# Performance work log

Hardware: AMD Instinct MI355X
Metric: run time of the kernel (lower is better)

The kernel has to match this reference:

```python
import jax, jax.numpy as jnp
import numpy as np

B, T, D, H, OUT = 4096, 48, 59, 256, 1


def _uni(k, shape, fan_in):
    s = 1.0 / np.sqrt(fan_in)
    return jax.random.uniform(k, shape, jnp.float32, -s, s)


def setup_inputs() -> dict:
    key = jax.random.key(0)
    ks = jax.random.split(key, 16)
    return {
        "x": jax.random.normal(ks[0], (B, T, D), jnp.float32),
        "mask": (jax.random.uniform(ks[1], (B, T, D)) < 0.7).astype(jnp.float32),
        "deltas": jax.random.uniform(ks[2], (B, T, D), jnp.float32) * 5.0,
        "last_obs": jax.random.normal(ks[3], (B, D), jnp.float32),
        "h": jax.random.normal(ks[4], (B, H), jnp.float32) * 0.1,
        "medians": jnp.zeros((D,), jnp.float32),  # medians_df=None -> zeros
        # Decay temp_decay_h (non-diag)
        "W_dh": _uni(ks[5], (H, D), D), "b_dh": jnp.zeros((H,), jnp.float32),
        # Decay temp_decay_x (diag, input==output)
        "W_dx": _uni(ks[6], (D, D), D), "b_dx": jnp.zeros((D,), jnp.float32),
        # hist: Linear(H, D)
        "hist_W": _uni(ks[7], (D, H), H), "hist_b": jnp.zeros((D,), jnp.float32),
        "feat_W": _uni(ks[8], (D, D), D), "feat_b": jnp.zeros((D,), jnp.float32),
        # weight_combine: Linear(2D, D)
        "wcomb_W": _uni(ks[9], (D, 2 * D), 2 * D), "wcomb_b": jnp.zeros((D,), jnp.float32),
        # Decay_obs linear (D, D)
        "wobs_W": _uni(ks[10], (D, D), D), "wobs_b": jnp.zeros((D,), jnp.float32),
        # GRUCell(2D, H)
        "W_ih": _uni(ks[11], (3 * H, 2 * D), 2 * D),
        "W_hh": _uni(ks[12], (3 * H, H), H),
        "b_ih": jnp.zeros((3 * H,), jnp.float32),
        "b_hh": jnp.zeros((3 * H,), jnp.float32),
        # classification: Linear(H, OUT)
        "cls_W": _uni(ks[13], (OUT, H), H), "cls_b": jnp.zeros((OUT,), jnp.float32),
    }


def reference(x, mask, deltas, last_obs, h, medians,
              W_dh, b_dh, W_dx, b_dx, hist_W, hist_b, feat_W, feat_b,
              wcomb_W, wcomb_b, wobs_W, wobs_b,
              W_ih, W_hh, b_ih, b_hh, cls_W, cls_b):
    Dn = x.shape[-1]
    Hn = h.shape[-1]
    eye = jnp.eye(Dn, dtype=x.dtype)

    # Decay_obs: sign-gated tanh weighting of (deltas - medians)
    dd = deltas - medians[None, None, :]
    wd = jnp.einsum('btd,ed->bte', dd, wobs_W) + wobs_b
    # relu(wd) + relu(-wd) == |wd|
    decay_factor = 0.5 * (1.0 - jnp.tanh(jnp.sign(dd) * jnp.abs(wd)))  # [B,T,D]

    dx_diag = jnp.diagonal(W_dx)          # diag decay: W * eye
    feat_Wm = feat_W * (1.0 - eye)

    def step(h, ins):
        x_t, m_t, d_t = ins               # each [B,D]
        gamma_h = jnp.exp(-jax.nn.relu(d_t @ W_dh.T + b_dh))   # [B,H]
        h = h * gamma_h
        x_h = h @ hist_W.T + hist_b                              # history estimate [B,D]
        x_r = m_t * x_t + (1.0 - m_t) * x_h                      # complemented input
        xu = x_r @ feat_Wm.T + feat_b
        gamma_x = jnp.exp(-jax.nn.relu(d_t * dx_diag + b_dx))    # diag decay [B,D]
        beta = jax.nn.sigmoid(
            jnp.concatenate([gamma_x, m_t], axis=-1) @ wcomb_W.T + wcomb_b)
        x_comb = beta * xu + (1.0 - beta) * x_h
        loss_t = jnp.sum(jnp.abs(x_t - x_comb) * m_t) / (jnp.sum(m_t) + 1e-5)
        x_imp_t = m_t * x_t + (1.0 - m_t) * x_comb
        # GRUCell with input concat([x_imp_t, m_t])
        gi = jnp.concatenate([x_imp_t, m_t], axis=-1) @ W_ih.T + b_ih
        gh = h @ W_hh.T + b_hh
        r = jax.nn.sigmoid(gi[:, :Hn] + gh[:, :Hn])
        z = jax.nn.sigmoid(gi[:, Hn:2 * Hn] + gh[:, Hn:2 * Hn])
        n = jnp.tanh(gi[:, 2 * Hn:] + r * gh[:, 2 * Hn:])
        h_new = (1.0 - z) * n + z * h
        return h_new, (x_imp_t, h_new, loss_t)

    xs = (x.transpose(1, 0, 2), mask.transpose(1, 0, 2), deltas.transpose(1, 0, 2))
    h_last, (x_imp, hs, losses) = jax.lax.scan(step, h, xs)
    x_imp = x_imp.transpose(1, 0, 2)          # [B,T,D]
    hidden_states = hs.transpose(1, 0, 2)     # [B,T,H]
    x_loss = jnp.sum(losses)
    y_out = h_last @ cls_W.T + cls_b          # dropout = identity at eval
    y_score = jax.nn.sigmoid(y_out)
    return x_imp, x_loss, hidden_states, y_out, y_score, decay_factor
```

## Files before the change

kernel.cpp:

```cpp
#include <hip/hip_runtime.h>
#include <math.h>

#define BATCH 4096
#define TT 48
#define DDIM 59
#define HHID 256
#define RR 16
#define NWG (BATCH/RR)
#define NTHR 512

typedef _Float16 f16;
typedef _Float16 f16x8 __attribute__((ext_vector_type(8)));
typedef float    f32x4 __attribute__((ext_vector_type(4)));

static constexpr size_t N_XIMP   = (size_t)BATCH*TT*DDIM;
static constexpr size_t OFF_LOSS = N_XIMP;
static constexpr size_t OFF_HS   = OFF_LOSS + 1;
static constexpr size_t N_HS     = (size_t)BATCH*TT*HHID;
static constexpr size_t OFF_YOUT = OFF_HS + N_HS;
static constexpr size_t OFF_YSC  = OFF_YOUT + BATCH;
static constexpr size_t OFF_DEC  = OFF_YSC + BATCH;

static constexpr size_t WOFF_GRU  = 0;
static constexpr size_t WOFF_DH   = 294912;
static constexpr size_t WOFF_HIST = 311296;
static constexpr size_t WOFF_FEAT = 327680;
static constexpr size_t WOFF_WC   = 331776;

__device__ __forceinline__ float sigm(float v){ return 1.f/(1.f+expf(-v)); }

__global__ __launch_bounds__(256) void decay_kernel(
    const float* __restrict__ deltas, const float* __restrict__ medians,
    const float* __restrict__ wobs_W, const float* __restrict__ wobs_b,
    float* __restrict__ out_decay)
{
  __shared__ float sW[DDIM][60];
  __shared__ float sb[64], smed[64];
  __shared__ float sdd[16][60];
  const int tid = threadIdx.x;
  for (int idx = tid; idx < DDIM*DDIM; idx += 256){
    int e = idx/DDIM, d = idx - e*DDIM;
    sW[e][d] = wobs_W[idx];
  }
  if (tid < DDIM){ sb[tid] = wobs_b[tid]; smed[tid] = medians[tid]; }
  __syncthreads();
  const size_t row0 = (size_t)blockIdx.x * 16;
  for (int idx = tid; idx < 16*DDIM; idx += 256){
    int r = idx/DDIM, d = idx - r*DDIM;
    sdd[r][d] = deltas[(row0+r)*DDIM + d] - smed[d];
  }
  __syncthreads();
  for (int idx = tid; idx < 16*DDIM; idx += 256){
    int r = idx/DDIM, e = idx - r*DDIM;
    float acc = sb[e];
    for (int d = 0; d < DDIM; d++) acc += sdd[r][d]*sW[e][d];
    float dd = sdd[r][e];
    float sg = (dd > 0.f) ? 1.f : ((dd < 0.f) ? -1.f : 0.f);
    out_decay[(row0+r)*DDIM + e] = 0.5f*(1.f - tanhf(sg*fabsf(acc)));
  }
}

__global__ __launch_bounds__(256) void conv_kernel(
    const float* __restrict__ W_dh, const float* __restrict__ hist_W,
    const float* __restrict__ feat_W, const float* __restrict__ wcomb_W,
    const float* __restrict__ W_ih, const float* __restrict__ W_hh,
    f16* __restrict__ ws)
{
  const int g  = blockIdx.x*4 + (threadIdx.x >> 6);
  const int l  = threadIdx.x & 63;
  const int nl = l & 15;
  const int kh = (l >> 4) * 8;
  f16x8 out;
  if (g < 576){
    int jb = g/36, s = g - jb*36;
    if (s < 24){
      int gate = s/12, kt = s - gate*12;
      int row  = gate*256 + jb*16 + nl;
      #pragma unroll
      for (int e = 0; e < 8; e++){
        int k = kt*32 + kh + e;
        float v = (k < 256) ? W_hh[(size_t)row*256 + k]
                : (k < 374) ? W_ih[(size_t)row*118 + (k-256)] : 0.f;
        out[e] = (f16)v;
      }
    } else if (s < 32){
      int kt = s - 24, row = 512 + jb*16 + nl;
      #pragma unroll
      for (int e = 0; e < 8; e++){
        int k = kt*32 + kh + e;
        out[e] = (f16)W_hh[(size_t)row*256 + k];
      }
    } else {
      int kt = s - 32, row = 512 + jb*16 + nl;
      #pragma unroll
      for (int e = 0; e < 8; e++){
        int k = kt*32 + kh + e;
        out[e] = (f16)((k < 118) ? W_ih[(size_t)row*118 + k] : 0.f);
      }
    }
    *(f16x8*)&ws[WOFF_GRU + (size_t)g*512 + l*8] = out;
  } else if (g < 608){
    int i = g - 576, nt = i >> 1, kt = i & 1;
    int row = nt*16 + nl;
    #pragma unroll
    for (int e = 0; e < 8; e++){
      int k = kt*32 + kh + e;
      out[e] = (f16)((k < 59) ? W_dh[(size_t)row*59 + k] : 0.f);
    }
    *(f16x8*)&ws[WOFF_DH + (size_t)i*512 + l*8] = out;
  } else if (g < 640){
    int i = g - 608, nt = i >> 3, kt = i & 7;
    int n = nt*16 + nl;
    #pragma unroll
    for (int e = 0; e < 8; e++){
      int k = kt*32 + kh + e;
      out[e] = (f16)((n < 59) ? hist_W[(size_t)n*256 + k] : 0.f);
    }
    *(f16x8*)&ws[WOFF_HIST + (size_t)i*512 + l*8] = out;
  } else if (g < 648){
    int i = g - 640, nt = i >> 1, kt = i & 1;
    int n = nt*16 + nl;
    #pragma unroll
    for (int e = 0; e < 8; e++){
      int k = kt*32 + kh + e;
      out[e] = (f16)((n < 59 && k < 59 && k != n) ? feat_W[(size_t)n*59 + k] : 0.f);
    }
    *(f16x8*)&ws[WOFF_FEAT + (size_t)i*512 + l*8] = out;
  } else {
    int i = g - 648, nt = i >> 2, kt = i & 3;
    int n = nt*16 + nl;
    #pragma unroll
    for (int e = 0; e < 8; e++){
      int k = kt*32 + kh + e;
      out[e] = (f16)((n < 59 && k < 118) ? wcomb_W[(size_t)n*118 + k] : 0.f);
    }
    *(f16x8*)&ws[WOFF_WC + (size_t)i*512 + l*8] = out;
  }
}

__global__ __launch_bounds__(NTHR, 1) void seq_kernel(
    const float* __restrict__ x, const float* __restrict__ mask,
    const float* __restrict__ deltas, const float* __restrict__ h0,
    const float* __restrict__ b_dh, const float* __restrict__ W_dx,
    const float* __restrict__ b_dx, const float* __restrict__ hist_b,
    const float* __restrict__ feat_b, const float* __restrict__ wcomb_b,
    const float* __restrict__ b_ih, const float* __restrict__ b_hh,
    const f16* __restrict__ wb,
    float* __restrict__ out_ximp, float* __restrict__ out_hs,
    float* __restrict__ ws_num, float* __restrict__ ws_den)
{
  __shared__ f16 Acat[16*392];
  __shared__ f16 Ad  [16*72];
  __shared__ f16 Axr [16*72];
  __shared__ f16 Agm [16*136];
  __shared__ float ssx[16*60], ssm[16*60], ssd[16*60];
  __shared__ float sxh[16*60], sxu[16*60], sbt[16*60];
  __shared__ float sh [16*260];
  __shared__ float sdiag[64], sbdx[64];
  __shared__ float sredN[8], sredD[8];

  const int tid = threadIdx.x;
  const int w   = tid >> 6;
  const int l   = tid & 63;
  const int nl  = l & 15;
  const int kh  = (l >> 4) * 8;
  const int mq  = (l >> 4) * 4;
  const int row0 = blockIdx.x * RR;

  const f16* Bgru  = wb + WOFF_GRU;
  const f16* Bdh   = wb + WOFF_DH;
  const f16* Bhist = wb + WOFF_HIST;
  const f16* Bfeat = wb + WOFF_FEAT;
  const f16* Bwc   = wb + WOFF_WC;

  if (tid < DDIM){ sdiag[tid] = W_dx[(size_t)tid*DDIM + tid]; sbdx[tid] = b_dx[tid]; }
  for (int idx = tid; idx < 16*18; idx += NTHR){
    int r = idx/18, c = idx - (idx/18)*18;
    Acat[r*392 + 374 + c] = (f16)0.f;
    Agm [r*136 + 118 + c] = (f16)0.f;
  }
  for (int idx = tid; idx < 16*13; idx += NTHR){
    int r = idx/13, c = idx - (idx/13)*13;
    Ad [r*72 + 59 + c] = (f16)0.f;
    Axr[r*72 + 59 + c] = (f16)0.f;
  }
  for (int idx = tid; idx < 16*256; idx += NTHR){
    int r = idx >> 8, j = idx & 255;
    sh[r*260 + j] = h0[(size_t)(row0+r)*HHID + j];
  }
  __syncthreads();

  for (int t = 0; t < TT; t++){
    for (int idx = tid; idx < 944; idx += NTHR){
      int r = idx/59, d = idx - r*59;
      size_t g = ((size_t)(row0+r)*TT + t)*DDIM + d;
      float xv = x[g], mv = mask[g], dv = deltas[g];
      ssx[r*60+d] = xv; ssm[r*60+d] = mv; ssd[r*60+d] = dv;
      Ad  [r*72 +d]      = (f16)dv;
      Agm [r*136+59+d]   = (f16)mv;
      Acat[r*392+315+d]  = (f16)mv;
    }
    __syncthreads();

    #pragma unroll
    for (int ii = 0; ii < 2; ii++){
      int nt = 2*w + ii;
      f32x4 acc = {0.f,0.f,0.f,0.f};
      #pragma unroll
      for (int kt = 0; kt < 2; kt++){
        f16x8 a = *(const f16x8*)&Ad[nl*72 + kt*32 + kh];
        f16x8 b = *(const f16x8*)&Bdh[(size_t)(nt*2+kt)*512 + l*8];
        acc = __builtin_amdgcn_mfma_f32_16x16x32_f16(a, b, acc, 0, 0, 0);
      }
      int n = nt*16 + nl;
      float bn = b_dh[n];
      #pragma unroll
      for (int q = 0; q < 4; q++){
        int m = mq + q;
        float gm = expf(-fmaxf(acc[q] + bn, 0.f));
        float hv = sh[m*260 + n] * gm;
        sh[m*260 + n] = hv;
        Acat[m*392 + n] = (f16)hv;
      }
    }
    __syncthreads();

    if (w < 4){
      int nt = w;
      f32x4 acc = {0.f,0.f,0.f,0.f};
      #pragma unroll
      for (int kt = 0; kt < 8; kt++){
        f16x8 a = *(const f16x8*)&Acat[nl*392 + kt*32 + kh];
        f16x8 b = *(const f16x8*)&Bhist[(size_t)(nt*8+kt)*512 + l*8];
        acc = __builtin_amdgcn_mfma_f32_16x16x32_f16(a, b, acc, 0, 0, 0);
      }
      int n = nt*16 + nl;
      if (n < DDIM){
        float hb = hist_b[n];
        #pragma unroll
        for (int q = 0; q < 4; q++) sxh[(mq+q)*60 + n] = acc[q] + hb;
      }
    } else {
      for (int idx = tid - 256; idx < 944; idx += 256){
        int r = idx/59, d = idx - r*59;
        float gx = expf(-fmaxf(ssd[r*60+d]*sdiag[d] + sbdx[d], 0.f));
        Agm[r*136 + d] = (f16)gx;
      }
    }
    __syncthreads();

    for (int idx = tid; idx < 944; idx += NTHR){
      int r = idx/59, d = idx - r*59;
      float m = ssm[r*60+d];
      float xr = m*ssx[r*60+d] + (1.f-m)*sxh[r*60+d];
      Axr[r*72+d] = (f16)xr;
    }
    __syncthreads();

    if (w < 4){
      int nt = w;
      f32x4 acc = {0.f,0.f,0.f,0.f};
      #pragma unroll
      for (int kt = 0; kt < 2; kt++){
        f16x8 a = *(const f16x8*)&Axr[nl*72 + kt*32 + kh];
        f16x8 b = *(const f16x8*)&Bfeat[(size_t)(nt*2+kt)*512 + l*8];
        acc = __builtin_amdgcn_mfma_f32_16x16x32_f16(a, b, acc, 0, 0, 0);
      }
      int n = nt*16 + nl;
      if (n < DDIM){
        float fb = feat_b[n];
        #pragma unroll
        for (int q = 0; q < 4; q++) sxu[(mq+q)*60 + n] = acc[q] + fb;
      }
    } else {
      int nt = w - 4;
      f32x4 acc = {0.f,0.f,0.f,0.f};
      #pragma unroll
      for (int kt = 0; kt < 4; kt++){
        f16x8 a = *(const f16x8*)&Agm[nl*136 + kt*32 + kh];
        f16x8 b = *(const f16x8*)&Bwc[(size_t)(nt*4+kt)*512 + l*8];
        acc = __builtin_amdgcn_mfma_f32_16x16x32_f16(a, b, acc, 0, 0, 0);
      }
      int n = nt*16 + nl;
      if (n < DDIM){
        float cb = wcomb_b[n];
        #pragma unroll
        for (int q = 0; q < 4; q++) sbt[(mq+q)*60 + n] = sigm(acc[q] + cb);
      }
    }
    __syncthreads();

    float lnum = 0.f, lden = 0.f;
    for (int idx = tid; idx < 944; idx += NTHR){
      int r = idx/59, i = idx - r*59;
      float xh = sxh[r*60+i], xu = sxu[r*60+i], bt = sbt[r*60+i];
      float xc = bt*xu + (1.f-bt)*xh;
      float m = ssm[r*60+i], xv = ssx[r*60+i];
      lnum += fabsf(xv - xc)*m;
      lden += m;
      float xi = m*xv + (1.f-m)*xc;
      Acat[r*392 + 256 + i] = (f16)xi;
      out_ximp[((size_t)(row0+r)*TT + t)*DDIM + i] = xi;
    }
    #pragma unroll
    for (int off = 32; off >= 1; off >>= 1){
      lnum += __shfl_xor(lnum, off);
      lden += __shfl_xor(lden, off);
    }
    if (l == 0){ sredN[w] = lnum; sredD[w] = lden; }
    __syncthreads();
    if (tid == 0){
      float a = 0.f, b = 0.f;
      #pragma unroll
      for (int k = 0; k < 8; k++){ a += sredN[k]; b += sredD[k]; }
      atomicAdd(&ws_num[t], a); atomicAdd(&ws_den[t], b);
    }

    #pragma unroll
    for (int jj = 0; jj < 2; jj++){
      int jb = 2*w + jj;
      const f16* Bb = Bgru + (size_t)jb*36*512;
      f32x4 ar  = {0.f,0.f,0.f,0.f};
      f32x4 az  = {0.f,0.f,0.f,0.f};
      f32x4 anh = {0.f,0.f,0.f,0.f};
      f32x4 ani = {0.f,0.f,0.f,0.f};
      #pragma unroll
      for (int kt = 0; kt < 12; kt++){
        f16x8 a  = *(const f16x8*)&Acat[nl*392 + kt*32 + kh];
        f16x8 br = *(const f16x8*)&Bb[(size_t)kt*512 + l*8];
        f16x8 bz = *(const f16x8*)&Bb[(size_t)(12+kt)*512 + l*8];
        ar = __builtin_amdgcn_mfma_f32_16x16x32_f16(a, br, ar, 0, 0, 0);
        az = __builtin_amdgcn_mfma_f32_16x16x32_f16(a, bz, az, 0, 0, 0);
        if (kt < 8){
          f16x8 bn = *(const f16x8*)&Bb[(size_t)(24+kt)*512 + l*8];
          anh = __builtin_amdgcn_mfma_f32_16x16x32_f16(a, bn, anh, 0, 0, 0);
        } else {
          f16x8 bn = *(const f16x8*)&Bb[(size_t)(32+kt-8)*512 + l*8];
          ani = __builtin_amdgcn_mfma_f32_16x16x32_f16(a, bn, ani, 0, 0, 0);
        }
      }
      int j = jb*16 + nl;
      float br_ = b_ih[j]       + b_hh[j];
      float bz_ = b_ih[256+j]   + b_hh[256+j];
      float bni = b_ih[512+j];
      float bnh = b_hh[512+j];
      #pragma unroll
      for (int q = 0; q < 4; q++){
        int m = mq + q;
        float rg = sigm(ar[q] + br_);
        float zg = sigm(az[q] + bz_);
        float ng = tanhf(ani[q] + bni + rg*(anh[q] + bnh));
        float hold = sh[m*260 + j];
        float hn = (1.f-zg)*ng + zg*hold;
        sh[m*260 + j] = hn;
        out_hs[((size_t)(row0+m)*TT + t)*HHID + j] = hn;
      }
    }
    __syncthreads();
  }
}

__global__ __launch_bounds__(256) void final_kernel(
    const float* __restrict__ hs, const float* __restrict__ cls_W,
    const float* __restrict__ cls_b, const float* __restrict__ ws_num,
    const float* __restrict__ ws_den, float* __restrict__ out)
{
  int b = blockIdx.x*256 + threadIdx.x;
  if (b < BATCH){
    const float* hr = hs + ((size_t)b*TT + (TT-1))*HHID;
    float acc = cls_b[0];
    for (int j = 0; j < HHID; j++) acc += hr[j]*cls_W[j];
    out[OFF_YOUT + b] = acc;
    out[OFF_YSC  + b] = sigm(acc);
  }
  if (blockIdx.x == 0 && threadIdx.x == 0){
    float s = 0.f;
    for (int tt = 0; tt < TT; tt++) s += ws_num[tt]/(ws_den[tt] + 1e-5f);
    out[OFF_LOSS] = s;
  }
}

extern "C" void kernel_launch(void* const* d_in, const int* in_sizes, int n_in,
                              void* d_out, int out_size, void* d_ws, size_t ws_size,
                              hipStream_t stream)
{
  const float* x       = (const float*)d_in[0];
  const float* mask_   = (const float*)d_in[1];
  const float* deltas  = (const float*)d_in[2];
  const float* h0      = (const float*)d_in[4];
  const float* medians = (const float*)d_in[5];
  const float* W_dh    = (const float*)d_in[6];
  const float* b_dh    = (const float*)d_in[7];
  const float* W_dx    = (const float*)d_in[8];
  const float* b_dx    = (const float*)d_in[9];
  const float* hist_W  = (const float*)d_in[10];
  const float* hist_b  = (const float*)d_in[11];
  const float* feat_W  = (const float*)d_in[12];
  const float* feat_b  = (const float*)d_in[13];
  const float* wcomb_W = (const float*)d_in[14];
  const float* wcomb_b = (const float*)d_in[15];
  const float* wobs_W  = (const float*)d_in[16];
  const float* wobs_b  = (const float*)d_in[17];
  const float* W_ih    = (const float*)d_in[18];
  const float* W_hh    = (const float*)d_in[19];
  const float* b_ih    = (const float*)d_in[20];
  const float* b_hh    = (const float*)d_in[21];
  const float* cls_W   = (const float*)d_in[22];
  const float* cls_b   = (const float*)d_in[23];

  float* out    = (float*)d_out;
  float* ws_num = (float*)d_ws;
  float* ws_den = ws_num + TT;
  f16*   wbase  = (f16*)((char*)d_ws + 512);

  hipMemsetAsync(d_ws, 0, 512, stream);

  conv_kernel<<<166, 256, 0, stream>>>(W_dh, hist_W, feat_W, wcomb_W,
                                       W_ih, W_hh, wbase);

  decay_kernel<<<BATCH*TT/16, 256, 0, stream>>>(deltas, medians, wobs_W, wobs_b,
                                                out + OFF_DEC);

  seq_kernel<<<NWG, NTHR, 0, stream>>>(x, mask_, deltas, h0,
      b_dh, W_dx, b_dx, hist_b, feat_b, wcomb_b, b_ih, b_hh, wbase,
      out , out + OFF_HS, ws_num, ws_den);

  final_kernel<<<BATCH/256, 256, 0, stream>>>(out + OFF_HS, cls_W, cls_b,
                                              ws_num, ws_den, out);
}
```

Before: 1.426 ms.

## Process 32 rows per workgroup, keep hidden state in registers, prefetch next timestep

Doubles the rows per workgroup so each weight fragment loaded from global memory feeds two MFMAs, halving per-row weight traffic in every per-step GEMM, especially the GRU. The hidden state moves from shared memory into per-lane registers, and biases are hoisted out of the time loop. The next timestep's x/mask/deltas are prefetched into registers while the current step computes, and intermediate shared buffers are shrunk to fp16 to fit. Risks: half as many workgroups (128) on a 256-CU part, so per-step latency may dominate; also more register pressure and extra fp16 rounding of x and the intermediates.

```diff
diff --git a/kernel.cpp b/kernel.cpp
--- a/kernel.cpp
+++ b/kernel.cpp
@@ -5,7 +5,7 @@
 #define TT 48
 #define DDIM 59
 #define HHID 256
-#define RR 16
+#define RR 32
 #define NWG (BATCH/RR)
 #define NTHR 512
 
@@ -149,13 +149,13 @@
     float* __restrict__ out_ximp, float* __restrict__ out_hs,
     float* __restrict__ ws_num, float* __restrict__ ws_den)
 {
-  __shared__ f16 Acat[16*392];
-  __shared__ f16 Ad  [16*72];
-  __shared__ f16 Axr [16*72];
-  __shared__ f16 Agm [16*136];
-  __shared__ float ssx[16*60], ssm[16*60], ssd[16*60];
-  __shared__ float sxh[16*60], sxu[16*60], sbt[16*60];
-  __shared__ float sh [16*260];
+  __shared__ f16 Acat[RR*392];
+  __shared__ f16 AdAxr[RR*72];
+  __shared__ f16 Agm [RR*136];
+  __shared__ f16 ssx [RR*60];
+  __shared__ f16 sxh [RR*60];
+  __shared__ f16 sxu [RR*60];
+  __shared__ f16 sbt [RR*60];
   __shared__ float sdiag[64], sbdx[64];
   __shared__ float sredN[8], sredD[8];
 
@@ -173,129 +173,197 @@
   const f16* Bfeat = wb + WOFF_FEAT;
   const f16* Bwc   = wb + WOFF_WC;
 
+  const int i0 = tid,          r0s = i0/59, d0s = i0 - r0s*59;
+  const int i1 = tid + 512,    r1s = i1/59, d1s = i1 - r1s*59;
+  const int i2 = tid + 1024,   r2s = i2/59, d2s = i2 - r2s*59;
+  const int i3 = tid + 1536,   r3s = i3/59, d3s = i3 - r3s*59;
+  const bool has3 = (i3 < RR*59);
+
+  const int nA = w*16 + nl;
+  const int nB = (w-4)*16 + nl;
+  const float hb_n = (w < 4 && nA < DDIM) ? hist_b[nA] : 0.f;
+  const float fb_n = (w < 4 && nA < DDIM) ? feat_b[nA] : 0.f;
+  const float cb_n = (w >= 4 && nB < DDIM) ? wcomb_b[nB] : 0.f;
+  float bdh_i[2], br_j[2], bz_j[2], bni_j[2], bnh_j[2];
+  #pragma unroll
+  for (int ii = 0; ii < 2; ii++){
+    int n = (2*w+ii)*16 + nl;
+    bdh_i[ii] = b_dh[n];
+    br_j[ii]  = b_ih[n]     + b_hh[n];
+    bz_j[ii]  = b_ih[256+n] + b_hh[256+n];
+    bni_j[ii] = b_ih[512+n];
+    bnh_j[ii] = b_hh[512+n];
+  }
+
   if (tid < DDIM){ sdiag[tid] = W_dx[(size_t)tid*DDIM + tid]; sbdx[tid] = b_dx[tid]; }
-  for (int idx = tid; idx < 16*18; idx += NTHR){
+  for (int idx = tid; idx < RR*18; idx += NTHR){
     int r = idx/18, c = idx - (idx/18)*18;
     Acat[r*392 + 374 + c] = (f16)0.f;
     Agm [r*136 + 118 + c] = (f16)0.f;
   }
-  for (int idx = tid; idx < 16*13; idx += NTHR){
+  for (int idx = tid; idx < RR*13; idx += NTHR){
     int r = idx/13, c = idx - (idx/13)*13;
-    Ad [r*72 + 59 + c] = (f16)0.f;
-    Axr[r*72 + 59 + c] = (f16)0.f;
-  }
-  for (int idx = tid; idx < 16*256; idx += NTHR){
-    int r = idx >> 8, j = idx & 255;
-    sh[r*260 + j] = h0[(size_t)(row0+r)*HHID + j];
+    AdAxr[r*72 + 59 + c] = (f16)0.f;
+  }
+
+  float hreg[2][2][4];
+  #pragma unroll
+  for (int mt = 0; mt < 2; mt++)
+    #pragma unroll
+    for (int ii = 0; ii < 2; ii++){
+      int n = (2*w+ii)*16 + nl;
+      #pragma unroll
+      for (int q = 0; q < 4; q++)
+        hreg[mt][ii][q] = h0[(size_t)(row0 + mt*16 + mq + q)*HHID + n];
+    }
+
+  float vx0,vm0,vd0, vx1,vm1,vd1, vx2,vm2,vd2, vx3=0.f,vm3=0.f,vd3=0.f;
+  {
+    size_t g0 = ((size_t)(row0+r0s)*TT)*DDIM + d0s;
+    size_t g1 = ((size_t)(row0+r1s)*TT)*DDIM + d1s;
+    size_t g2 = ((size_t)(row0+r2s)*TT)*DDIM + d2s;
+    vx0 = x[g0]; vm0 = mask[g0]; vd0 = deltas[g0];
+    vx1 = x[g1]; vm1 = mask[g1]; vd1 = deltas[g1];
+    vx2 = x[g2]; vm2 = mask[g2]; vd2 = deltas[g2];
+    if (has3){
+      size_t g3 = ((size_t)(row0+r3s)*TT)*DDIM + d3s;
+      vx3 = x[g3]; vm3 = mask[g3]; vd3 = deltas[g3];
+    }
   }
   __syncthreads();
 
   for (int t = 0; t < TT; t++){
-    for (int idx = tid; idx < 944; idx += NTHR){
-      int r = idx/59, d = idx - r*59;
-      size_t g = ((size_t)(row0+r)*TT + t)*DDIM + d;
-      float xv = x[g], mv = mask[g], dv = deltas[g];
-      ssx[r*60+d] = xv; ssm[r*60+d] = mv; ssd[r*60+d] = dv;
-      Ad  [r*72 +d]      = (f16)dv;
-      Agm [r*136+59+d]   = (f16)mv;
-      Acat[r*392+315+d]  = (f16)mv;
-    }
-    __syncthreads();
+    ssx[r0s*60+d0s] = (f16)vx0; AdAxr[r0s*72+d0s] = (f16)vd0;
+    Agm[r0s*136+59+d0s] = (f16)vm0; Acat[r0s*392+315+d0s] = (f16)vm0;
+    ssx[r1s*60+d1s] = (f16)vx1; AdAxr[r1s*72+d1s] = (f16)vd1;
+    Agm[r1s*136+59+d1s] = (f16)vm1; Acat[r1s*392+315+d1s] = (f16)vm1;
+    ssx[r2s*60+d2s] = (f16)vx2; AdAxr[r2s*72+d2s] = (f16)vd2;
+    Agm[r2s*136+59+d2s] = (f16)vm2; Acat[r2s*392+315+d2s] = (f16)vm2;
+    if (has3){
+      ssx[r3s*60+d3s] = (f16)vx3; AdAxr[r3s*72+d3s] = (f16)vd3;
+      Agm[r3s*136+59+d3s] = (f16)vm3; Acat[r3s*392+315+d3s] = (f16)vm3;
+    }
+    __syncthreads();
+
+    if (t + 1 < TT){
+      size_t g0 = ((size_t)(row0+r0s)*TT + (t+1))*DDIM + d0s;
+      size_t g1 = ((size_t)(row0+r1s)*TT + (t+1))*DDIM + d1s;
+      size_t g2 = ((size_t)(row0+r2s)*TT + (t+1))*DDIM + d2s;
+      vx0 = x[g0]; vm0 = mask[g0]; vd0 = deltas[g0];
+      vx1 = x[g1]; vm1 = mask[g1]; vd1 = deltas[g1];
+      vx2 = x[g2]; vm2 = mask[g2]; vd2 = deltas[g2];
+      if (has3){
+        size_t g3 = ((size_t)(row0+r3s)*TT + (t+1))*DDIM + d3s;
+        vx3 = x[g3]; vm3 = mask[g3]; vd3 = deltas[g3];
+      }
+    }
 
     #pragma unroll
     for (int ii = 0; ii < 2; ii++){
       int nt = 2*w + ii;
-      f32x4 acc = {0.f,0.f,0.f,0.f};
+      f32x4 acc0 = {0.f,0.f,0.f,0.f}, acc1 = {0.f,0.f,0.f,0.f};
       #pragma unroll
       for (int kt = 0; kt < 2; kt++){
-        f16x8 a = *(const f16x8*)&Ad[nl*72 + kt*32 + kh];
-        f16x8 b = *(const f16x8*)&Bdh[(size_t)(nt*2+kt)*512 + l*8];
-        acc = __builtin_amdgcn_mfma_f32_16x16x32_f16(a, b, acc, 0, 0, 0);
+        f16x8 b  = *(const f16x8*)&Bdh[(size_t)(nt*2+kt)*512 + l*8];
+        f16x8 a0 = *(const f16x8*)&AdAxr[nl*72 + kt*32 + kh];
+        f16x8 a1 = *(const f16x8*)&AdAxr[(16+nl)*72 + kt*32 + kh];
+        acc0 = __builtin_amdgcn_mfma_f32_16x16x32_f16(a0, b, acc0, 0, 0, 0);
+        acc1 = __builtin_amdgcn_mfma_f32_16x16x32_f16(a1, b, acc1, 0, 0, 0);
       }
       int n = nt*16 + nl;
-      float bn = b_dh[n];
       #pragma unroll
       for (int q = 0; q < 4; q++){
-        int m = mq + q;
-        float gm = expf(-fmaxf(acc[q] + bn, 0.f));
-        float hv = sh[m*260 + n] * gm;
-        sh[m*260 + n] = hv;
-        Acat[m*392 + n] = (f16)hv;
+        float g0f = expf(-fmaxf(acc0[q] + bdh_i[ii], 0.f));
+        float g1f = expf(-fmaxf(acc1[q] + bdh_i[ii], 0.f));
+        float h0v = hreg[0][ii][q] * g0f;
+        float h1v = hreg[1][ii][q] * g1f;
+        hreg[0][ii][q] = h0v;
+        hreg[1][ii][q] = h1v;
+        Acat[(mq+q)*392 + n]      = (f16)h0v;
+        Acat[(16+mq+q)*392 + n]   = (f16)h1v;
       }
     }
     __syncthreads();
 
     if (w < 4){
-      int nt = w;
-      f32x4 acc = {0.f,0.f,0.f,0.f};
+      f32x4 acc0 = {0.f,0.f,0.f,0.f}, acc1 = {0.f,0.f,0.f,0.f};
       #pragma unroll
       for (int kt = 0; kt < 8; kt++){
-        f16x8 a = *(const f16x8*)&Acat[nl*392 + kt*32 + kh];
-        f16x8 b = *(const f16x8*)&Bhist[(size_t)(nt*8+kt)*512 + l*8];
-        acc = __builtin_amdgcn_mfma_f32_16x16x32_f16(a, b, acc, 0, 0, 0);
-      }
-      int n = nt*16 + nl;
-      if (n < DDIM){
-        float hb = hist_b[n];
+        f16x8 b  = *(const f16x8*)&Bhist[(size_t)(w*8+kt)*512 + l*8];
+        f16x8 a0 = *(const f16x8*)&Acat[nl*392 + kt*32 + kh];
+        f16x8 a1 = *(const f16x8*)&Acat[(16+nl)*392 + kt*32 + kh];
+        acc0 = __builtin_amdgcn_mfma_f32_16x16x32_f16(a0, b, acc0, 0, 0, 0);
+        acc1 = __builtin_amdgcn_mfma_f32_16x16x32_f16(a1, b, acc1, 0, 0, 0);
+      }
+      if (nA < DDIM){
         #pragma unroll
-        for (int q = 0; q < 4; q++) sxh[(mq+q)*60 + n] = acc[q] + hb;
+        for (int q = 0; q < 4; q++){
+          sxh[(mq+q)*60 + nA]    = (f16)(acc0[q] + hb_n);
+          sxh[(16+mq+q)*60 + nA] = (f16)(acc1[q] + hb_n);
+        }
       }
     } else {
-      for (int idx = tid - 256; idx < 944; idx += 256){
+      for (int idx = tid - 256; idx < RR*59; idx += 256){
         int r = idx/59, d = idx - r*59;
-        float gx = expf(-fmaxf(ssd[r*60+d]*sdiag[d] + sbdx[d], 0.f));
+        float dv = (float)AdAxr[r*72 + d];
+        float gx = expf(-fmaxf(dv*sdiag[d] + sbdx[d], 0.f));
         Agm[r*136 + d] = (f16)gx;
       }
     }
     __syncthreads();
 
-    for (int idx = tid; idx < 944; idx += NTHR){
+    for (int idx = tid; idx < RR*59; idx += NTHR){
       int r = idx/59, d = idx - r*59;
-      float m = ssm[r*60+d];
-      float xr = m*ssx[r*60+d] + (1.f-m)*sxh[r*60+d];
-      Axr[r*72+d] = (f16)xr;
+      float m  = (float)Acat[r*392 + 315 + d];
+      float xr = m*(float)ssx[r*60+d] + (1.f-m)*(float)sxh[r*60+d];
+      AdAxr[r*72+d] = (f16)xr;
     }
     __syncthreads();
 
     if (w < 4){
-      int nt = w;
-      f32x4 acc = {0.f,0.f,0.f,0.f};
+      f32x4 acc0 = {0.f,0.f,0.f,0.f}, acc1 = {0.f,0.f,0.f,0.f};
       #pragma unroll
       for (int kt = 0; kt < 2; kt++){
-        f16x8 a = *(const f16x8*)&Axr[nl*72 + kt*32 + kh];
-        f16x8 b = *(const f16x8*)&Bfeat[(size_t)(nt*2+kt)*512 + l*8];
-        acc = __builtin_amdgcn_mfma_f32_16x16x32_f16(a, b, acc, 0, 0, 0);
-      }
-      int n = nt*16 + nl;
-      if (n < DDIM){
-        float fb = feat_b[n];
+        f16x8 b  = *(const f16x8*)&Bfeat[(size_t)(w*2+kt)*512 + l*8];
+        f16x8 a0 = *(const f16x8*)&AdAxr[nl*72 + kt*32 + kh];
+        f16x8 a1 = *(const f16x8*)&AdAxr[(16+nl)*72 + kt*32 + kh];
+        acc0 = __builtin_amdgcn_mfma_f32_16x16x32_f16(a0, b, acc0, 0, 0, 0);
+        acc1 = __builtin_amdgcn_mfma_f32_16x16x32_f16(a1, b, acc1, 0, 0, 0);
+      }
+      if (nA < DDIM){
         #pragma unroll
-        for (int q = 0; q < 4; q++) sxu[(mq+q)*60 + n] = acc[q] + fb;
+        for (int q = 0; q < 4; q++){
+          sxu[(mq+q)*60 + nA]    = (f16)(acc0[q] + fb_n);
+          sxu[(16+mq+q)*60 + nA] = (f16)(acc1[q] + fb_n);
+        }
       }
     } else {
-      int nt = w - 4;
-      f32x4 acc = {0.f,0.f,0.f,0.f};
+      f32x4 acc0 = {0.f,0.f,0.f,0.f}, acc1 = {0.f,0.f,0.f,0.f};
       #pragma unroll
       for (int kt = 0; kt < 4; kt++){
-        f16x8 a = *(const f16x8*)&Agm[nl*136 + kt*32 + kh];
-        f16x8 b = *(const f16x8*)&Bwc[(size_t)(nt*4+kt)*512 + l*8];
-        acc = __builtin_amdgcn_mfma_f32_16x16x32_f16(a, b, acc, 0, 0, 0);
-      }
-      int n = nt*16 + nl;
-      if (n < DDIM){
-        float cb = wcomb_b[n];
+        f16x8 b  = *(const f16x8*)&Bwc[(size_t)((w-4)*4+kt)*512 + l*8];
+        f16x8 a0 = *(const f16x8*)&Agm[nl*136 + kt*32 + kh];
+        f16x8 a1 = *(const f16x8*)&Agm[(16+nl)*136 + kt*32 + kh];
+        acc0 = __builtin_amdgcn_mfma_f32_16x16x32_f16(a0, b, acc0, 0, 0, 0);
+        acc1 = __builtin_amdgcn_mfma_f32_16x16x32_f16(a1, b, acc1, 0, 0, 0);
+      }
+      if (nB < DDIM){
         #pragma unroll
-        for (int q = 0; q < 4; q++) sbt[(mq+q)*60 + n] = sigm(acc[q] + cb);
+        for (int q = 0; q < 4; q++){
+          sbt[(mq+q)*60 + nB]    = (f16)sigm(acc0[q] + cb_n);
+          sbt[(16+mq+q)*60 + nB] = (f16)sigm(acc1[q] + cb_n);
+        }
       }
     }
     __syncthreads();
 
     float lnum = 0.f, lden = 0.f;
-    for (int idx = tid; idx < 944; idx += NTHR){
+    for (int idx = tid; idx < RR*59; idx += NTHR){
       int r = idx/59, i = idx - r*59;
-      float xh = sxh[r*60+i], xu = sxu[r*60+i], bt = sbt[r*60+i];
+      float xh = (float)sxh[r*60+i], xu = (float)sxu[r*60+i], bt = (float)sbt[r*60+i];
       float xc = bt*xu + (1.f-bt)*xh;
-      float m = ssm[r*60+i], xv = ssx[r*60+i];
+      float m = (float)Acat[r*392 + 315 + i];
+      float xv = (float)ssx[r*60+i];
       lnum += fabsf(xv - xc)*m;
       lden += m;
       float xi = m*xv + (1.f-m)*xc;
@@ -320,40 +388,44 @@
     for (int jj = 0; jj < 2; jj++){
       int jb = 2*w + jj;
       const f16* Bb = Bgru + (size_t)jb*36*512;
-      f32x4 ar  = {0.f,0.f,0.f,0.f};
-      f32x4 az  = {0.f,0.f,0.f,0.f};
-      f32x4 anh = {0.f,0.f,0.f,0.f};
-      f32x4 ani = {0.f,0.f,0.f,0.f};
+      f32x4 ar0={0,0,0,0}, az0={0,0,0,0}, anh0={0,0,0,0}, ani0={0,0,0,0};
+      f32x4 ar1={0,0,0,0}, az1={0,0,0,0}, anh1={0,0,0,0}, ani1={0,0,0,0};
       #pragma unroll
       for (int kt = 0; kt < 12; kt++){
-        f16x8 a  = *(const f16x8*)&Acat[nl*392 + kt*32 + kh];
+        f16x8 a0 = *(const f16x8*)&Acat[nl*392 + kt*32 + kh];
+        f16x8 a1 = *(const f16x8*)&Acat[(16+nl)*392 + kt*32 + kh];
         f16x8 br = *(const f16x8*)&Bb[(size_t)kt*512 + l*8];
         f16x8 bz = *(const f16x8*)&Bb[(size_t)(12+kt)*512 + l*8];
-        ar = __builtin_amdgcn_mfma_f32_16x16x32_f16(a, br, ar, 0, 0, 0);
-        az = __builtin_amdgcn_mfma_f32_16x16x32_f16(a, bz, az, 0, 0, 0);
+        ar0 = __builtin_amdgcn_mfma_f32_16x16x32_f16(a0, br, ar0, 0, 0, 0);
+        ar1 = __builtin_amdgcn_mfma_f32_16x16x32_f16(a1, br, ar1, 0, 0, 0);
+        az0 = __builtin_amdgcn_mfma_f32_16x16x32_f16(a0, bz, az0, 0, 0, 0);
+        az1 = __builtin_amdgcn_mfma_f32_16x16x32_f16(a1, bz, az1, 0, 0, 0);
         if (kt < 8){
           f16x8 bn = *(const f16x8*)&Bb[(size_t)(24+kt)*512 + l*8];
-          anh = __builtin_amdgcn_mfma_f32_16x16x32_f16(a, bn, anh, 0, 0, 0);
+          anh0 = __builtin_amdgcn_mfma_f32_16x16x32_f16(a0, bn, anh0, 0, 0, 0);
+          anh1 = __builtin_amdgcn_mfma_f32_16x16x32_f16(a1, bn, anh1, 0, 0, 0);
         } else {
           f16x8 bn = *(const f16x8*)&Bb[(size_t)(32+kt-8)*512 + l*8];
-          ani = __builtin_amdgcn_mfma_f32_16x16x32_f16(a, bn, ani, 0, 0, 0);
+          ani0 = __builtin_amdgcn_mfma_f32_16x16x32_f16(a0, bn, ani0, 0, 0, 0);
+          ani1 = __builtin_amdgcn_mfma_f32_16x16x32_f16(a1, bn, ani1, 0, 0, 0);
         }
       }
       int j = jb*16 + nl;
-      float br_ = b_ih[j]       + b_hh[j];
-      float bz_ = b_ih[256+j]   + b_hh[256+j];
-      float bni = b_ih[512+j];
-      float bnh = b_hh[512+j];
       #pragma unroll
       for (int q = 0; q < 4; q++){
-        int m = mq + q;
-        float rg = sigm(ar[q] + br_);
-        float zg = sigm(az[q] + bz_);
-        float ng = tanhf(ani[q] + bni + rg*(anh[q] + bnh));
-        float hold = sh[m*260 + j];
-        float hn = (1.f-zg)*ng + zg*hold;
-        sh[m*260 + j] = hn;
-        out_hs[((size_t)(row0+m)*TT + t)*HHID + j] = hn;
+        float rg = sigm(ar0[q] + br_j[jj]);
+        float zg = sigm(az0[q] + bz_j[jj]);
+        float ng = tanhf(ani0[q] + bni_j[jj] + rg*(anh0[q] + bnh_j[jj]));
+        float hn = (1.f-zg)*ng + zg*hreg[0][jj][q];
+        hreg[0][jj][q] = hn;
+        out_hs[((size_t)(row0+mq+q)*TT + t)*HHID + j] = hn;
+
+        rg = sigm(ar1[q] + br_j[jj]);
+        zg = sigm(az1[q] + bz_j[jj]);
+        ng = tanhf(ani1[q] + bni_j[jj] + rg*(anh1[q] + bnh_j[jj]));
+        hn = (1.f-zg)*ng + zg*hreg[1][jj][q];
+        hreg[1][jj][q] = hn;
+        out_hs[((size_t)(row0+16+mq+q)*TT + t)*HHID + j] = hn;
       }
     }
     __syncthreads();
```

After: 2.605 ms. +82.6%, slower.

## Double block width, prefetch next step inputs, and split GRU matmul across phases

Applied to the files above, without the earlier changes.

Raises the sequential kernel to 1024 threads so each wave owns one 16-column GRU/decay tile. The h-dependent part of the GRU gates (first 8 K-tiles) now runs in the same phase as the hist matmul, and only the x_imp/mask K-tiles remain after the loss step. The next timestep's x/mask/deltas are register-prefetched, and biases are hoisted out of the loop. Scratch buffers are shrunk to fp16, and gamma_x is computed alongside the decay phase, removing one barrier phase. The cost is higher register pressure from the live partial accumulators and extra fp16 rounding of intermediate x values.

```diff
diff --git a/kernel.cpp b/kernel.cpp
--- a/kernel.cpp
+++ b/kernel.cpp
@@ -7,7 +7,7 @@
 #define HHID 256
 #define RR 16
 #define NWG (BATCH/RR)
-#define NTHR 512
+#define NTHR 1024
 
 typedef _Float16 f16;
 typedef _Float16 f16x8 __attribute__((ext_vector_type(8)));
@@ -138,7 +138,7 @@
   }
 }
 
-__global__ __launch_bounds__(NTHR, 1) void seq_kernel(
+__global__ __launch_bounds__(NTHR) void seq_kernel(
     const float* __restrict__ x, const float* __restrict__ mask,
     const float* __restrict__ deltas, const float* __restrict__ h0,
     const float* __restrict__ b_dh, const float* __restrict__ W_dx,
@@ -149,15 +149,16 @@
     float* __restrict__ out_ximp, float* __restrict__ out_hs,
     float* __restrict__ ws_num, float* __restrict__ ws_den)
 {
-  __shared__ f16 Acat[16*392];
-  __shared__ f16 Ad  [16*72];
-  __shared__ f16 Axr [16*72];
-  __shared__ f16 Agm [16*136];
-  __shared__ float ssx[16*60], ssm[16*60], ssd[16*60];
-  __shared__ float sxh[16*60], sxu[16*60], sbt[16*60];
-  __shared__ float sh [16*260];
+  __shared__ f16 Acat[RR*392];
+  __shared__ f16 AdAxr[RR*72];
+  __shared__ f16 Agm [RR*136];
+  __shared__ f16 ssx [RR*60];
+  __shared__ f16 sxh [RR*60];
+  __shared__ f16 sxu [RR*60];
+  __shared__ f16 sbt [RR*60];
+  __shared__ float sh [RR*260];
   __shared__ float sdiag[64], sbdx[64];
-  __shared__ float sredN[8], sredD[8];
+  __shared__ float sredN[16], sredD[16];
 
   const int tid = threadIdx.x;
   const int w   = tid >> 6;
@@ -172,135 +173,156 @@
   const f16* Bhist = wb + WOFF_HIST;
   const f16* Bfeat = wb + WOFF_FEAT;
   const f16* Bwc   = wb + WOFF_WC;
+  const f16* Bb    = Bgru + (size_t)w*36*512;
+
+  const bool hasS = (tid < RR*DDIM);
+  const int r0s = tid/59, d0s = tid - r0s*59;
+
+  const int nG = w*16 + nl;
+  const float bdh_n = b_dh[nG];
+  const float br_j  = b_ih[nG]     + b_hh[nG];
+  const float bz_j  = b_ih[256+nG] + b_hh[256+nG];
+  const float bni_j = b_ih[512+nG];
+  const float bnh_j = b_hh[512+nG];
+  const int nA = w*16 + nl;
+  const int nB = (w-4)*16 + nl;
+  const float hb_n = (w < 4 && nA < DDIM) ? hist_b[nA] : 0.f;
+  const float fb_n = (w < 4 && nA < DDIM) ? feat_b[nA] : 0.f;
+  const float cb_n = (w >= 4 && w < 8 && nB < DDIM) ? wcomb_b[nB] : 0.f;
 
   if (tid < DDIM){ sdiag[tid] = W_dx[(size_t)tid*DDIM + tid]; sbdx[tid] = b_dx[tid]; }
-  for (int idx = tid; idx < 16*18; idx += NTHR){
+  for (int idx = tid; idx < RR*18; idx += NTHR){
     int r = idx/18, c = idx - (idx/18)*18;
     Acat[r*392 + 374 + c] = (f16)0.f;
     Agm [r*136 + 118 + c] = (f16)0.f;
   }
-  for (int idx = tid; idx < 16*13; idx += NTHR){
+  for (int idx = tid; idx < RR*13; idx += NTHR){
     int r = idx/13, c = idx - (idx/13)*13;
-    Ad [r*72 + 59 + c] = (f16)0.f;
-    Axr[r*72 + 59 + c] = (f16)0.f;
-  }
-  for (int idx = tid; idx < 16*256; idx += NTHR){
+    AdAxr[r*72 + 59 + c] = (f16)0.f;
+  }
+  for (int idx = tid; idx < RR*HHID; idx += NTHR){
     int r = idx >> 8, j = idx & 255;
     sh[r*260 + j] = h0[(size_t)(row0+r)*HHID + j];
   }
+
+  float vx0 = 0.f, vm0 = 0.f, vd0 = 0.f;
+  if (hasS){
+    size_t g0 = ((size_t)(row0+r0s)*TT)*DDIM + d0s;
+    vx0 = x[g0]; vm0 = mask[g0]; vd0 = deltas[g0];
+  }
   __syncthreads();
 
   for (int t = 0; t < TT; t++){
-    for (int idx = tid; idx < 944; idx += NTHR){
-      int r = idx/59, d = idx - r*59;
-      size_t g = ((size_t)(row0+r)*TT + t)*DDIM + d;
-      float xv = x[g], mv = mask[g], dv = deltas[g];
-      ssx[r*60+d] = xv; ssm[r*60+d] = mv; ssd[r*60+d] = dv;
-      Ad  [r*72 +d]      = (f16)dv;
-      Agm [r*136+59+d]   = (f16)mv;
-      Acat[r*392+315+d]  = (f16)mv;
-    }
-    __syncthreads();
-
-    #pragma unroll
-    for (int ii = 0; ii < 2; ii++){
-      int nt = 2*w + ii;
+    if (hasS){
+      ssx[r0s*60+d0s] = (f16)vx0;
+      AdAxr[r0s*72+d0s] = (f16)vd0;
+      Agm[r0s*136+59+d0s] = (f16)vm0;
+      Acat[r0s*392+315+d0s] = (f16)vm0;
+    }
+    __syncthreads();
+
+    if (t + 1 < TT && hasS){
+      size_t g0 = ((size_t)(row0+r0s)*TT + (t+1))*DDIM + d0s;
+      vx0 = x[g0]; vm0 = mask[g0]; vd0 = deltas[g0];
+    }
+
+    {
       f32x4 acc = {0.f,0.f,0.f,0.f};
       #pragma unroll
       for (int kt = 0; kt < 2; kt++){
-        f16x8 a = *(const f16x8*)&Ad[nl*72 + kt*32 + kh];
-        f16x8 b = *(const f16x8*)&Bdh[(size_t)(nt*2+kt)*512 + l*8];
+        f16x8 a = *(const f16x8*)&AdAxr[nl*72 + kt*32 + kh];
+        f16x8 b = *(const f16x8*)&Bdh[(size_t)(w*2+kt)*512 + l*8];
         acc = __builtin_amdgcn_mfma_f32_16x16x32_f16(a, b, acc, 0, 0, 0);
       }
-      int n = nt*16 + nl;
-      float bn = b_dh[n];
       #pragma unroll
       for (int q = 0; q < 4; q++){
-        int m = mq + q;
-        float gm = expf(-fmaxf(acc[q] + bn, 0.f));
-        float hv = sh[m*260 + n] * gm;
-        sh[m*260 + n] = hv;
-        Acat[m*392 + n] = (f16)hv;
-      }
+        float gm = expf(-fmaxf(acc[q] + bdh_n, 0.f));
+        float hv = sh[(mq+q)*260 + nG] * gm;
+        sh[(mq+q)*260 + nG] = hv;
+        Acat[(mq+q)*392 + nG] = (f16)hv;
+      }
+      if (hasS){
+        float dv = (float)AdAxr[r0s*72 + d0s];
+        float gx = expf(-fmaxf(dv*sdiag[d0s] + sbdx[d0s], 0.f));
+        Agm[r0s*136 + d0s] = (f16)gx;
+      }
+    }
+    __syncthreads();
+
+    f32x4 gr = {0.f,0.f,0.f,0.f}, gz = {0.f,0.f,0.f,0.f}, gnh = {0.f,0.f,0.f,0.f};
+    {
+      #pragma unroll
+      for (int kt = 0; kt < 8; kt++){
+        f16x8 a  = *(const f16x8*)&Acat[nl*392 + kt*32 + kh];
+        f16x8 br = *(const f16x8*)&Bb[(size_t)kt*512 + l*8];
+        f16x8 bz = *(const f16x8*)&Bb[(size_t)(12+kt)*512 + l*8];
+        f16x8 bn = *(const f16x8*)&Bb[(size_t)(24+kt)*512 + l*8];
+        gr  = __builtin_amdgcn_mfma_f32_16x16x32_f16(a, br, gr, 0, 0, 0);
+        gz  = __builtin_amdgcn_mfma_f32_16x16x32_f16(a, bz, gz, 0, 0, 0);
+        gnh = __builtin_amdgcn_mfma_f32_16x16x32_f16(a, bn, gnh, 0, 0, 0);
+      }
+      if (w < 4){
+        f32x4 acc = {0.f,0.f,0.f,0.f};
+        #pragma unroll
+        for (int kt = 0; kt < 8; kt++){
+          f16x8 a = *(const f16x8*)&Acat[nl*392 + kt*32 + kh];
+          f16x8 b = *(const f16x8*)&Bhist[(size_t)(w*8+kt)*512 + l*8];
+          acc = __builtin_amdgcn_mfma_f32_16x16x32_f16(a, b, acc, 0, 0, 0);
+        }
+        if (nA < DDIM){
+          #pragma unroll
+          for (int q = 0; q < 4; q++) sxh[(mq+q)*60 + nA] = (f16)(acc[q] + hb_n);
+        }
+      } else if (w < 8){
+        f32x4 acc = {0.f,0.f,0.f,0.f};
+        #pragma unroll
+        for (int kt = 0; kt < 4; kt++){
+          f16x8 a = *(const f16x8*)&Agm[nl*136 + kt*32 + kh];
+          f16x8 b = *(const f16x8*)&Bwc[(size_t)((w-4)*4+kt)*512 + l*8];
+          acc = __builtin_amdgcn_mfma_f32_16x16x32_f16(a, b, acc, 0, 0, 0);
+        }
+        if (nB < DDIM){
+          #pragma unroll
+          for (int q = 0; q < 4; q++) sbt[(mq+q)*60 + nB] = (f16)sigm(acc[q] + cb_n);
+        }
+      }
+    }
+    __syncthreads();
+
+    if (hasS){
+      float m  = (float)Acat[r0s*392 + 315 + d0s];
+      float xr = m*(float)ssx[r0s*60+d0s] + (1.f-m)*(float)sxh[r0s*60+d0s];
+      AdAxr[r0s*72+d0s] = (f16)xr;
     }
     __syncthreads();
 
     if (w < 4){
-      int nt = w;
       f32x4 acc = {0.f,0.f,0.f,0.f};
       #pragma unroll
-      for (int kt = 0; kt < 8; kt++){
-        f16x8 a = *(const f16x8*)&Acat[nl*392 + kt*32 + kh];
-        f16x8 b = *(const f16x8*)&Bhist[(size_t)(nt*8+kt)*512 + l*8];
+      for (int kt = 0; kt < 2; kt++){
+        f16x8 a = *(const f16x8*)&AdAxr[nl*72 + kt*32 + kh];
+        f16x8 b = *(const f16x8*)&Bfeat[(size_t)(w*2+kt)*512 + l*8];
         acc = __builtin_amdgcn_mfma_f32_16x16x32_f16(a, b, acc, 0, 0, 0);
       }
-      int n = nt*16 + nl;
-      if (n < DDIM){
-        float hb = hist_b[n];
+      if (nA < DDIM){
         #pragma unroll
-        for (int q = 0; q < 4; q++) sxh[(mq+q)*60 + n] = acc[q] + hb;
-      }
-    } else {
-      for (int idx = tid - 256; idx < 944; idx += 256){
-        int r = idx/59, d = idx - r*59;
-        float gx = expf(-fmaxf(ssd[r*60+d]*sdiag[d] + sbdx[d], 0.f));
-        Agm[r*136 + d] = (f16)gx;
-      }
-    }
-    __syncthreads();
-
-    for (int idx = tid; idx < 944; idx += NTHR){
-      int r = idx/59, d = idx - r*59;
-      float m = ssm[r*60+d];
-      float xr = m*ssx[r*60+d] + (1.f-m)*sxh[r*60+d];
-      Axr[r*72+d] = (f16)xr;
-    }
-    __syncthreads();
-
-    if (w < 4){
-      int nt = w;
-      f32x4 acc = {0.f,0.f,0.f,0.f};
-      #pragma unroll
-      for (int kt = 0; kt < 2; kt++){
-        f16x8 a = *(const f16x8*)&Axr[nl*72 + kt*32 + kh];
-        f16x8 b = *(const f16x8*)&Bfeat[(size_t)(nt*2+kt)*512 + l*8];
-        acc = __builtin_amdgcn_mfma_f32_16x16x32_f16(a, b, acc, 0, 0, 0);
-      }
-      int n = nt*16 + nl;
-      if (n < DDIM){
-        float fb = feat_b[n];
-        #pragma unroll
-        for (int q = 0; q < 4; q++) sxu[(mq+q)*60 + n] = acc[q] + fb;
-      }
-    } else {
-      int nt = w - 4;
-      f32x4 acc = {0.f,0.f,0.f,0.f};
-      #pragma unroll
-      for (int kt = 0; kt < 4; kt++){
-        f16x8 a = *(const f16x8*)&Agm[nl*136 + kt*32 + kh];
-        f16x8 b = *(const f16x8*)&Bwc[(size_t)(nt*4+kt)*512 + l*8];
-        acc = __builtin_amdgcn_mfma_f32_16x16x32_f16(a, b, acc, 0, 0, 0);
-      }
-      int n = nt*16 + nl;
-      if (n < DDIM){
-        float cb = wcomb_b[n];
-        #pragma unroll
-        for (int q = 0; q < 4; q++) sbt[(mq+q)*60 + n] = sigm(acc[q] + cb);
+        for (int q = 0; q < 4; q++) sxu[(mq+q)*60 + nA] = (f16)(acc[q] + fb_n);
       }
     }
     __syncthreads();
 
     float lnum = 0.f, lden = 0.f;
-    for (int idx = tid; idx < 944; idx += NTHR){
-      int r = idx/59, i = idx - r*59;
-      float xh = sxh[r*60+i], xu = sxu[r*60+i], bt = sbt[r*60+i];
+    if (hasS){
+      float xh = (float)sxh[r0s*60+d0s], xu = (float)sxu[r0s*60+d0s];
+      float bt = (float)sbt[r0s*60+d0s];
       float xc = bt*xu + (1.f-bt)*xh;
-      float m = ssm[r*60+i], xv = ssx[r*60+i];
-      lnum += fabsf(xv - xc)*m;
-      lden += m;
+      float m  = (float)Acat[r0s*392 + 315 + d0s];
+      float xv = (float)ssx[r0s*60+d0s];
+      lnum = fabsf(xv - xc)*m;
+      lden = m;
       float xi = m*xv + (1.f-m)*xc;
-      Acat[r*392 + 256 + i] = (f16)xi;
-      out_ximp[((size_t)(row0+r)*TT + t)*DDIM + i] = xi;
+      Acat[r0s*392 + 256 + d0s] = (f16)xi;
+      out_ximp[((size_t)(row0+r0s)*TT + t)*DDIM + d0s] = xi;
     }
     #pragma unroll
     for (int off = 32; off >= 1; off >>= 1){
@@ -312,48 +334,31 @@
     if (tid == 0){
       float a = 0.f, b = 0.f;
       #pragma unroll
-      for (int k = 0; k < 8; k++){ a += sredN[k]; b += sredD[k]; }
+      for (int k = 0; k < 16; k++){ a += sredN[k]; b += sredD[k]; }
       atomicAdd(&ws_num[t], a); atomicAdd(&ws_den[t], b);
     }
 
-    #pragma unroll
-    for (int jj = 0; jj < 2; jj++){
-      int jb = 2*w + jj;
-      const f16* Bb = Bgru + (size_t)jb*36*512;
-      f32x4 ar  = {0.f,0.f,0.f,0.f};
-      f32x4 az  = {0.f,0.f,0.f,0.f};
-      f32x4 anh = {0.f,0.f,0.f,0.f};
-      f32x4 ani = {0.f,0.f,0.f,0.f};
-      #pragma unroll
-      for (int kt = 0; kt < 12; kt++){
+    {
+      f32x4 gni = {0.f,0.f,0.f,0.f};
+      #pragma unroll
+      for (int kt = 8; kt < 12; kt++){
         f16x8 a  = *(const f16x8*)&Acat[nl*392 + kt*32 + kh];
         f16x8 br = *(const f16x8*)&Bb[(size_t)kt*512 + l*8];
         f16x8 bz = *(const f16x8*)&Bb[(size_t)(12+kt)*512 + l*8];
-        ar = __builtin_amdgcn_mfma_f32_16x16x32_f16(a, br, ar, 0, 0, 0);
-        az = __builtin_amdgcn_mfma_f32_16x16x32_f16(a, bz, az, 0, 0, 0);
-        if (kt < 8){
-          f16x8 bn = *(const f16x8*)&Bb[(size_t)(24+kt)*512 + l*8];
-          anh = __builtin_amdgcn_mfma_f32_16x16x32_f16(a, bn, anh, 0, 0, 0);
-        } else {
-          f16x8 bn = *(const f16x8*)&Bb[(size_t)(32+kt-8)*512 + l*8];
-          ani = __builtin_amdgcn_mfma_f32_16x16x32_f16(a, bn, ani, 0, 0, 0);
-        }
-      }
-      int j = jb*16 + nl;
-      float br_ = b_ih[j]       + b_hh[j];
-      float bz_ = b_ih[256+j]   + b_hh[256+j];
-      float bni = b_ih[512+j];
-      float bnh = b_hh[512+j];
+        f16x8 bn = *(const f16x8*)&Bb[(size_t)(32+kt-8)*512 + l*8];
+        gr  = __builtin_amdgcn_mfma_f32_16x16x32_f16(a, br, gr, 0, 0, 0);
+        gz  = __builtin_amdgcn_mfma_f32_16x16x32_f16(a, bz, gz, 0, 0, 0);
+        gni = __builtin_amdgcn_mfma_f32_16x16x32_f16(a, bn, gni, 0, 0, 0);
+      }
       #pragma unroll
       for (int q = 0; q < 4; q++){
-        int m = mq + q;
-        float rg = sigm(ar[q] + br_);
-        float zg = sigm(az[q] + bz_);
-        float ng = tanhf(ani[q] + bni + rg*(anh[q] + bnh));
-        float hold = sh[m*260 + j];
+        float rg = sigm(gr[q] + br_j);
+        float zg = sigm(gz[q] + bz_j);
+        float ng = tanhf(gni[q] + bni_j + rg*(gnh[q] + bnh_j));
+        float hold = sh[(mq+q)*260 + nG];
         float hn = (1.f-zg)*ng + zg*hold;
-        sh[m*260 + j] = hn;
-        out_hs[((size_t)(row0+m)*TT + t)*HHID + j] = hn;
+        sh[(mq+q)*260 + nG] = hn;
+        out_hs[((size_t)(row0+mq+q)*TT + t)*HHID + nG] = hn;
       }
     }
     __syncthreads();
```

New measurement: 1.727 ms. 21.0% more time.
